# Optimization experiments

Hardware: AMD Instinct MI355X
Metric: run time of the kernel (lower is better)

Reference implementation:

```python
import jax, jax.numpy as jnp
import numpy as np

SPIXELS = 1000
CLASSES = 21


def setup_inputs() -> dict:
    key = jax.random.key(0)
    k1, k2, k3, k4 = jax.random.split(key, 4)
    B, H, W = 8, 512, 512
    pred = jax.random.normal(k1, (B, CLASSES, H, W), dtype=jnp.float32)
    Laplace_W_c = jax.random.normal(k2, (B, SPIXELS, SPIXELS), dtype=jnp.float32)
    Laplace_L_c = jax.random.normal(k3, (B, SPIXELS, SPIXELS), dtype=jnp.float32)
    image_spiex = jax.random.randint(k4, (B, H, W), 0, SPIXELS, dtype=jnp.int32)
    return {"pred": pred, "Laplace_W_c": Laplace_W_c, "Laplace_L_c": Laplace_L_c, "image_spiex": image_spiex}


def reference(pred, Laplace_W_c, Laplace_L_c, image_spiex):
    B, _, H, W = pred.shape
    P = H * W
    # Faithful to original: permute(0,2,3,1) then reshape to [B, class_num, H*W]
    pred_r = jnp.transpose(pred, (0, 2, 3, 1)).reshape(B, CLASSES, P)  # [B, C, P]
    seg = image_spiex.reshape(B, P)  # [B, P] superpixel ids
    # result[b, c, s] = sum_{p: seg[b,p]==s} pred_r[b, c, p]  -- the bmm(pred, one_hot_mask)
    # expressed as an efficient segment-sum instead of materializing [B, P, SPIXELS].
    seg_sum = jax.vmap(
        lambda x, ids: jax.ops.segment_sum(x, ids, num_segments=SPIXELS)
    )(jnp.transpose(pred_r, (0, 2, 1)), seg)  # [B, S, C]
    result = jnp.transpose(seg_sum, (0, 2, 1))  # [B, C, S]
    # mask.sum() = count of (b, p, s) with seg[b,p] == s, i.e. pixels with valid ids
    mask_sum = jnp.sum(((seg >= 0) & (seg < SPIXELS)).astype(pred.dtype))
    result = result / (mask_sum + 1e-16)
    # trace(R @ L @ R^T) per batch, fused
    traces = jnp.einsum('bcs,bst,bct->b', result, Laplace_L_c, result)  # [B]
    loss = (2.0 / jnp.linalg.norm(Laplace_W_c)) * traces
    return jnp.mean(loss)
```

## Files before the change

### kernel.cpp

```cpp
#include <hip/hip_runtime.h>
#include <hip/hip_bf16.h>

#define SPIX 1000
#define NCLS 21
#define PP (512*512)
#define NB_IMG 8
#define EPB (NCLS*PP)

#define FWIN 32768
#define BLKS_PER_B (EPB / FWIN)
#define DUMP 1000

#define R_OFF   0
#define TR_OFF  (NB_IMG*NCLS*SPIX)
#define NS_OFF  (TR_OFF + NB_IMG)
#define CNT_OFF (NS_OFF + 1)
#define CTR_OFF (CNT_OFF + 1)
#define WS_FLOATS (CTR_OFF + 1)

__device__ __forceinline__ void fatomic_add(float* p, float v) {
    unsafeAtomicAdd(p, v);
}

__global__ __launch_bounds__(512, 4) void scatter_kernel(const float* __restrict__ pred,
                                                         const int* __restrict__ seg,
                                                         const float* __restrict__ W,
                                                         float* __restrict__ Rout,
                                                         float* __restrict__ ns,
                                                         float* __restrict__ cnt) {
    if (blockIdx.y == NB_IMG) {
        if (blockIdx.x < 128) {
            const float4* W4 = (const float4*)W;
            const int n4 = (NB_IMG * SPIX * SPIX) / 4;
            float s = 0.f;
            for (int i = blockIdx.x * 512 + threadIdx.x; i < n4; i += 128 * 512) {
                float4 v = W4[i];
                s += v.x*v.x + v.y*v.y + v.z*v.z + v.w*v.w;
            }
            #pragma unroll
            for (int off = 32; off; off >>= 1) s += __shfl_xor(s, off);
            if ((threadIdx.x & 63) == 0) fatomic_add(ns, s);
        } else {
            const int4* s4 = (const int4*)seg;
            const int n4 = (NB_IMG * PP) / 4;
            int c = 0;
            for (int i = (blockIdx.x - 128) * 512 + threadIdx.x; i < n4; i += 40 * 512) {
                int4 v = s4[i];
                c += ((unsigned)v.x < SPIX) + ((unsigned)v.y < SPIX) + ((unsigned)v.z < SPIX) + ((unsigned)v.w < SPIX);
            }
            float f = (float)c;
            #pragma unroll
            for (int off = 32; off; off >>= 1) f += __shfl_xor(f, off);
            if ((threadIdx.x & 63) == 0) fatomic_add(cnt, f);
        }
        return;
    }
    __shared__ float          Rw[8][1024];
    __shared__ unsigned short Mk[8][1024];
    const int b    = blockIdx.y;
    const int tid  = threadIdx.x;
    const int wave = tid >> 6;
    const unsigned lane = tid & 63;
    const unsigned f0 = (unsigned)blockIdx.x * FWIN;
    const unsigned c0 = f0 >> 18;
    const unsigned p0 = f0 & (PP - 1);

    for (int i = tid; i < 8 * 1024; i += 512) ((float*)Rw)[i] = 0.f;
    __syncthreads();

    volatile float*          vR = Rw[wave];
    volatile unsigned short* vM = Mk[wave];
    float* aR = (float*)Rw[wave];

    const float* pb   = pred + (size_t)b * EPB;
    const int*   segb = seg + (size_t)b * PP + p0;

    for (int it = 0; it < FWIN / (512 * 4); ++it) {
        const int e0 = (it * 512 + tid) * 4;
        int4 sv = *(const int4*)(segb + e0);
        const unsigned fk0 = f0 + (unsigned)e0;
        int sA[4]; float vA[4];
        #pragma unroll
        for (int k = 0; k < 4; ++k) {
            unsigned fk = fk0 + k;
            unsigned sp = fk / 21u;
            unsigned ch = fk - sp * 21u;
            vA[k] = pb[(ch << 18) + sp];
            int s = (&sv.x)[k];
            sA[k] = ((unsigned)s < SPIX) ? s : DUMP;
        }
        #pragma unroll
        for (int i = 0; i < 3; ++i)
            #pragma unroll
            for (int j = i + 1; j < 4; ++j) {
                bool e = (sA[j] == sA[i]) && (sA[i] != DUMP);
                vA[i] += e ? vA[j] : 0.f;
                sA[j]  = e ? DUMP  : sA[j];
            }
        #pragma unroll
        for (int k = 0; k < 4; ++k) vM[sA[k]] = (unsigned short)lane;
        unsigned short rd[4];
        #pragma unroll
        for (int k = 0; k < 4; ++k) rd[k] = vM[sA[k]];
        float od[4];
        #pragma unroll
        for (int k = 0; k < 4; ++k) od[k] = vR[sA[k]];
        #pragma unroll
        for (int k = 0; k < 4; ++k) {
            bool win = (rd[k] == (unsigned short)lane);
            vR[win ? sA[k] : DUMP] = od[k] + vA[k];
        }
        asm volatile("" ::: "memory");
        #pragma unroll
        for (int k = 0; k < 4; ++k) {
            if (rd[k] != (unsigned short)lane) fatomic_add(&aR[sA[k]], vA[k]);
        }
    }
    __syncthreads();

    float* Rb = Rout + (size_t)b * NCLS * SPIX + (size_t)c0 * SPIX;
    for (int i = tid; i < SPIX; i += 512) {
        float a = 0.f;
        #pragma unroll
        for (int w = 0; w < 8; ++w) a += Rw[w][i];
        fatomic_add(&Rb[i], a);
    }
}

__global__ __launch_bounds__(512) void trace_kernel(const float* __restrict__ L,
                                                    const float* __restrict__ R,
                                                    float* __restrict__ traces,
                                                    const float* __restrict__ ns,
                                                    const float* __restrict__ cnt,
                                                    unsigned* __restrict__ ctr,
                                                    float* __restrict__ out) {
    __shared__ float Rl[NCLS * SPIX];
    const int b = blockIdx.y;
    const float* Rb = R + (size_t)b * NCLS * SPIX;
    for (int i = threadIdx.x; i < NCLS * SPIX; i += 512) Rl[i] = Rb[i];
    __syncthreads();

    const int wave = threadIdx.x >> 6;
    const int lane = threadIdx.x & 63;
    const float* Lb = L + (size_t)b * SPIX * SPIX;

    const int s0 = (blockIdx.x * 8 + wave) * 4;
    bool val[4];
    const float4* Lr[4];
    #pragma unroll
    for (int r = 0; r < 4; ++r) {
        int sr = s0 + r;
        val[r] = sr < SPIX;
        Lr[r] = (const float4*)(Lb + (size_t)(val[r] ? sr : (SPIX - 1)) * SPIX);
    }

    float acc[4][NCLS];
    #pragma unroll
    for (int r = 0; r < 4; ++r)
        #pragma unroll
        for (int c = 0; c < NCLS; ++c) acc[r][c] = 0.f;

    #pragma unroll
    for (int it = 0; it < 4; ++it) {
        int idx = it * 64 + lane;
        if (idx < SPIX / 4) {
            float4 l[4];
            #pragma unroll
            for (int r = 0; r < 4; ++r)
                l[r] = val[r] ? Lr[r][idx] : make_float4(0.f, 0.f, 0.f, 0.f);
            #pragma unroll
            for (int c = 0; c < NCLS; ++c) {
                float4 rr = *(const float4*)&Rl[c * SPIX + idx * 4];
                #pragma unroll
                for (int r = 0; r < 4; ++r)
                    acc[r][c] += l[r].x * rr.x + l[r].y * rr.y + l[r].z * rr.z + l[r].w * rr.w;
            }
        }
    }

    float partial = 0.f;
    #pragma unroll
    for (int c = 0; c < NCLS; ++c)
        #pragma unroll
        for (int r = 0; r < 4; ++r)
            if (val[r]) partial += Rl[c * SPIX + s0 + r] * acc[r][c];

    #pragma unroll
    for (int off = 32; off; off >>= 1) partial += __shfl_xor(partial, off);
    if (lane == 0) fatomic_add(&traces[b], partial);

    __syncthreads();
    if (threadIdx.x == 0) {
        __threadfence();
        unsigned old = atomicAdd(ctr, 1u);
        if (old == 32u * NB_IMG - 1u) {
            __threadfence();
            float t = 0.f;
            #pragma unroll
            for (int i = 0; i < NB_IMG; ++i)
                t += __hip_atomic_load(&traces[i], __ATOMIC_RELAXED, __HIP_MEMORY_SCOPE_AGENT);
            float denom = cnt[0] + 1e-16f;
            out[0] = (2.f / sqrtf(ns[0])) * t / (denom * denom) / (float)NB_IMG;
        }
    }
}

extern "C" void kernel_launch(void* const* d_in, const int* in_sizes, int n_in,
                              void* d_out, int out_size, void* d_ws, size_t ws_size,
                              hipStream_t stream) {
    const float* pred = (const float*)d_in[0];
    const float* Wc   = (const float*)d_in[1];
    const float* Lc   = (const float*)d_in[2];
    const int*   seg  = (const int*)d_in[3];
    float* ws = (float*)d_ws;
    float* out = (float*)d_out;

    hipMemsetAsync(d_ws, 0, WS_FLOATS * sizeof(float), stream);

    scatter_kernel<<<dim3(BLKS_PER_B, NB_IMG + 1), 512, 0, stream>>>(
        pred, seg, Wc, ws + R_OFF, ws + NS_OFF, ws + CNT_OFF);

    trace_kernel<<<dim3(32, NB_IMG), 512, 0, stream>>>(
        Lc, ws + R_OFF, ws + TR_OFF, ws + NS_OFF, ws + CNT_OFF,
        (unsigned*)(ws + CTR_OFF), out);
}
```

Measured before the change: 159.3 us.

## Widen per-thread scatter batch to eight elements with second-round LDS conflict resolution

Each thread now handles eight elements per iteration instead of four. The per-element divide by 21 is replaced with an incremental channel/position counter, and duplicate ids within a thread are merged across all eight elements. A second round of mark-and-check in LDS resolves write collisions before falling back to LDS atomics, so fewer atomic adds should be issued. The cost is more LDS traffic and more registers per iteration, which may lower occupancy.

New measurement: 189.0 us. +18.6%, slower.

```diff
diff --git a/kernel.cpp b/kernel.cpp
--- a/kernel.cpp
+++ b/kernel.cpp
@@ -9,7 +9,9 @@
 
 #define FWIN 32768
 #define BLKS_PER_B (EPB / FWIN)
-#define DUMP 1000
+#define DUMP  1000
+#define DUMP2 1008
+#define KE 8
 
 #define R_OFF   0
 #define TR_OFF  (NB_IMG*NCLS*SPIX)
@@ -60,7 +62,7 @@
     const int b    = blockIdx.y;
     const int tid  = threadIdx.x;
     const int wave = tid >> 6;
-    const unsigned lane = tid & 63;
+    const unsigned short lane = (unsigned short)(tid & 63);
     const unsigned f0 = (unsigned)blockIdx.x * FWIN;
     const unsigned c0 = f0 >> 18;
     const unsigned p0 = f0 & (PP - 1);
@@ -75,45 +77,65 @@
     const float* pb   = pred + (size_t)b * EPB;
     const int*   segb = seg + (size_t)b * PP + p0;
 
-    for (int it = 0; it < FWIN / (512 * 4); ++it) {
-        const int e0 = (it * 512 + tid) * 4;
-        int4 sv = *(const int4*)(segb + e0);
-        const unsigned fk0 = f0 + (unsigned)e0;
-        int sA[4]; float vA[4];
-        #pragma unroll
-        for (int k = 0; k < 4; ++k) {
-            unsigned fk = fk0 + k;
+    for (int it = 0; it < FWIN / (512 * KE); ++it) {
+        const int e0 = (it * 512 + tid) * KE;
+        int4 sv0 = *(const int4*)(segb + e0);
+        int4 sv1 = *(const int4*)(segb + e0 + 4);
+        int sA[KE]; float vA[KE];
+        {
+            unsigned fk = f0 + (unsigned)e0;
             unsigned sp = fk / 21u;
             unsigned ch = fk - sp * 21u;
-            vA[k] = pb[(ch << 18) + sp];
-            int s = (&sv.x)[k];
-            sA[k] = ((unsigned)s < SPIX) ? s : DUMP;
-        }
-        #pragma unroll
-        for (int i = 0; i < 3; ++i)
-            #pragma unroll
-            for (int j = i + 1; j < 4; ++j) {
-                bool e = (sA[j] == sA[i]) && (sA[i] != DUMP);
+            #pragma unroll
+            for (int k = 0; k < KE; ++k) {
+                vA[k] = pb[(ch << 18) + sp];
+                int s = (k < 4) ? (&sv0.x)[k] : (&sv1.x)[k - 4];
+                sA[k] = ((unsigned)s < SPIX) ? s : DUMP;
+                ch++;
+                bool c21 = (ch == 21u);
+                sp += c21 ? 1u : 0u;
+                ch  = c21 ? 0u : ch;
+            }
+        }
+        #pragma unroll
+        for (int i = 0; i < KE - 1; ++i)
+            #pragma unroll
+            for (int j = i + 1; j < KE; ++j) {
+                bool e = (sA[j] == sA[i]);
                 vA[i] += e ? vA[j] : 0.f;
                 sA[j]  = e ? DUMP  : sA[j];
             }
         #pragma unroll
-        for (int k = 0; k < 4; ++k) vM[sA[k]] = (unsigned short)lane;
-        unsigned short rd[4];
-        #pragma unroll
-        for (int k = 0; k < 4; ++k) rd[k] = vM[sA[k]];
-        float od[4];
-        #pragma unroll
-        for (int k = 0; k < 4; ++k) od[k] = vR[sA[k]];
-        #pragma unroll
-        for (int k = 0; k < 4; ++k) {
-            bool win = (rd[k] == (unsigned short)lane);
-            vR[win ? sA[k] : DUMP] = od[k] + vA[k];
+        for (int k = 0; k < KE; ++k) vM[sA[k]] = lane;
+        unsigned short rd[KE];
+        #pragma unroll
+        for (int k = 0; k < KE; ++k) rd[k] = vM[sA[k]];
+        float od[KE];
+        #pragma unroll
+        for (int k = 0; k < KE; ++k) od[k] = vR[sA[k]];
+        bool lose1[KE];
+        #pragma unroll
+        for (int k = 0; k < KE; ++k) {
+            lose1[k] = (rd[k] != lane);
+            vR[lose1[k] ? DUMP : sA[k]] = od[k] + vA[k];
+        }
+        #pragma unroll
+        for (int k = 0; k < KE; ++k) vM[lose1[k] ? sA[k] : DUMP2] = lane;
+        unsigned short rd2[KE];
+        #pragma unroll
+        for (int k = 0; k < KE; ++k) rd2[k] = vM[lose1[k] ? sA[k] : DUMP2];
+        float od2[KE];
+        #pragma unroll
+        for (int k = 0; k < KE; ++k) od2[k] = vR[lose1[k] ? sA[k] : DUMP];
+        #pragma unroll
+        for (int k = 0; k < KE; ++k) {
+            bool w2 = lose1[k] && (rd2[k] == lane);
+            vR[w2 ? sA[k] : DUMP] = od2[k] + vA[k];
         }
         asm volatile("" ::: "memory");
         #pragma unroll
-        for (int k = 0; k < 4; ++k) {
-            if (rd[k] != (unsigned short)lane) fatomic_add(&aR[sA[k]], vA[k]);
+        for (int k = 0; k < KE; ++k) {
+            if (lose1[k] && rd2[k] != lane) fatomic_add(&aR[sA[k]], vA[k]);
         }
     }
     __syncthreads();
```
